# Performance work log

Hardware: AMD Instinct MI355X
Metric: run time of the kernel (lower is better)

Reference implementation:

```python
import jax, jax.numpy as jnp
import numpy as np

N = 50000
E = 800000
DIN = 128
DOUT = 128
T = 4  # number of edge types: onset, consecutive, during, rest


def setup_inputs() -> dict:
    key = jax.random.key(0)
    ks = jax.random.split(key, 12)
    s = 1.0 / np.sqrt(DIN)
    inp = {
        "x": jax.random.normal(ks[0], (N, DIN), dtype=jnp.float32),
        "edge_index": jax.random.randint(ks[1], (2, E), 0, N, dtype=jnp.int32),
        "edge_type": jax.random.randint(ks[2], (E,), 0, T, dtype=jnp.int32),
        # stacked per-etype parameters of ResGatedGraphConv
        "Wk": jax.random.uniform(ks[3], (T, DIN, DOUT), jnp.float32, -s, s),
        "bk": jax.random.uniform(ks[4], (T, DOUT), jnp.float32, -s, s),
        "Wq": jax.random.uniform(ks[5], (T, DIN, DOUT), jnp.float32, -s, s),
        "bq": jax.random.uniform(ks[6], (T, DOUT), jnp.float32, -s, s),
        "Wv": jax.random.uniform(ks[7], (T, DIN, DOUT), jnp.float32, -s, s),
        "bv": jax.random.uniform(ks[8], (T, DOUT), jnp.float32, -s, s),
        "Ws": jax.random.uniform(ks[9], (T, DIN, DOUT), jnp.float32, -s, s),
        "b": jax.random.uniform(ks[10], (T, DOUT), jnp.float32, -s, s),
    }
    return inp


def reference(x, edge_index, edge_type, Wk, bk, Wq, bq, Wv, bv, Ws, b):
    # PyG ResGatedGraphConv per edge type t, with edges masked to that type:
    #   out_i = sum_{j->i, type==t} sigmoid(k_i + q_j) * v_j + Ws_t x_i + b_t
    # followed by mean over edge types ('mean' reduction).
    src = edge_index[0]  # j (message source)
    dst = edge_index[1]  # i (message target)
    n = x.shape[0]
    outs = []
    for t in range(T):
        k = x @ Wk[t] + bk[t]  # [N, DOUT]
        q = x @ Wq[t] + bq[t]
        v = x @ Wv[t] + bv[t]
        eta = jax.nn.sigmoid(k[dst] + q[src])        # [E, DOUT]
        msg = eta * v[src]                            # [E, DOUT]
        msg = jnp.where((edge_type == t)[:, None], msg, 0.0)
        agg = jax.ops.segment_sum(msg, dst, num_segments=n)
        outs.append(agg + x @ Ws[t] + b[t])
    return jnp.mean(jnp.stack(outs, axis=0), axis=0)  # [N, DOUT]
```

## Files before the change

### kernel.cpp

```cpp
#include <hip/hip_runtime.h>

typedef unsigned short u16;
typedef unsigned int u32;
typedef __attribute__((ext_vector_type(8))) short bf16x8;
typedef __attribute__((ext_vector_type(4))) float f32x4;
typedef __attribute__((ext_vector_type(2))) float f32x2;
typedef __attribute__((ext_vector_type(4))) u16 u16x4;
typedef __attribute__((ext_vector_type(2))) u32 u32x2;
typedef __attribute__((ext_vector_type(4), aligned(4))) u32 u32x4a;
typedef __attribute__((ext_vector_type(2), aligned(4))) u32 u32x2a;

#define DIM 128
#define ROWB 2304
#define QV_SPAN 384
#define K_OFF 1536
#define S_OFF 2048
#define AS1C(p) ((const __attribute__((address_space(1))) void*)(p))
#define AS3P(p) ((__attribute__((address_space(3))) void*)(p))

#define QKSCALE -1.44269504088896341f

#if defined(__has_builtin)
#if __has_builtin(__builtin_amdgcn_exp2f)
#define EXP2(x) __builtin_amdgcn_exp2f(x)
#endif
#endif
#ifndef EXP2
extern "C" __device__ float __ocml_exp2_f32(float);
#define EXP2(x) __ocml_exp2_f32(x)
#endif

__device__ __forceinline__ u32 f2bf(float f){
  u32 x = __float_as_uint(f);
  return (x + 0x7fffu + ((x >> 16) & 1u)) >> 16;
}
__device__ __forceinline__ float bf2f(u16 u){
  return __uint_as_float(((u32)u) << 16);
}

__global__ __launch_bounds__(256) void prep_kernel(
    const float* __restrict__ x, u16* __restrict__ xb,
    const int* __restrict__ dst, int* __restrict__ cnt, int* __restrict__ rank,
    const float* __restrict__ Wk, const float* __restrict__ bk,
    const float* __restrict__ Wq, const float* __restrict__ bq,
    const float* __restrict__ Wv, const float* __restrict__ bv,
    const float* __restrict__ Ws, const float* __restrict__ bb,
    u16* __restrict__ WcatT, float* __restrict__ biascat,
    int T, int N, int E, int rows){
  int id = blockIdx.x * 256 + threadIdx.x;
  if (id < E){
    rank[id] = atomicAdd(&cnt[dst[id]], 1);
    return;
  }
  id -= E;
  int total_w = (3 * T + 1) * DIM * DIM;
  if (id < total_w){
    int kk = id & (DIM - 1);
    int c  = id >> 7;
    int nt = c >> 7;
    int j  = c & (DIM - 1);
    float wv, bvv;
    if (nt < T)        { wv = Wq[(nt*DIM + kk)*DIM + j] * QKSCALE;       bvv = bq[nt*DIM + j] * QKSCALE; }
    else if (nt < 2*T) { wv = Wv[((nt-T)*DIM + kk)*DIM + j];             bvv = bv[(nt-T)*DIM + j]; }
    else if (nt < 3*T) { wv = Wk[((nt-2*T)*DIM + kk)*DIM + j] * QKSCALE; bvv = bk[(nt-2*T)*DIM + j] * QKSCALE; }
    else {
      float s = 0.f, sb = 0.f;
      for (int t = 0; t < T; ++t){ s += Ws[(t*DIM + kk)*DIM + j]; sb += bb[t*DIM + j]; }
      wv = s / (float)T; bvv = sb / (float)T;
    }
    WcatT[(size_t)c * DIM + kk] = (u16)f2bf(wv);
    if (kk == 0) biascat[c] = bvv;
    return;
  }
  id -= total_w;
  int total_cast = rows * (DIM / 4);
  if (id < total_cast){
    int el = id * 4;
    int node = el >> 7;
    u32x2 pk;
    if (node < N){
      f32x4 v = *(const f32x4*)(x + el);
      pk.x = f2bf(v.x) | (f2bf(v.y) << 16);
      pk.y = f2bf(v.z) | (f2bf(v.w) << 16);
    } else { pk.x = 0u; pk.y = 0u; }
    *(u32x2*)(xb + el) = pk;
  }
}

__global__ __launch_bounds__(256) void scan1_kernel(const int* __restrict__ cnt,
                                                    int* __restrict__ offs,
                                                    int* __restrict__ bsum, int n){
  __shared__ int wsum[4];
  const int tid = threadIdx.x;
  const int lane = tid & 63, wave = tid >> 6;
  const int base = blockIdx.x * 2048 + tid * 8;
  int v[8]; int tot = 0;
#pragma unroll
  for (int j = 0; j < 8; ++j){
    int idx = base + j;
    int val = (idx < n) ? cnt[idx] : 0;
    v[j] = val; tot += val;
  }
  int incl = tot;
#pragma unroll
  for (int d = 1; d < 64; d <<= 1){
    int u = __shfl_up(incl, d, 64);
    if (lane >= d) incl += u;
  }
  if (lane == 63) wsum[wave] = incl;
  __syncthreads();
  int wbase = 0;
#pragma unroll
  for (int w = 0; w < 4; ++w) if (w < wave) wbase += wsum[w];
  int excl = wbase + incl - tot;
  if (tid == 255) bsum[blockIdx.x] = wbase + incl;
#pragma unroll
  for (int j = 0; j < 8; ++j){
    int idx = base + j;
    if (idx < n) offs[idx] = excl;
    excl += v[j];
  }
}

__global__ __launch_bounds__(64) void scan2_kernel(const int* __restrict__ bsum,
                                                   int* __restrict__ boffs, int nb,
                                                   int* __restrict__ packed, int E){
  int lane = threadIdx.x;
  int v = (lane < nb) ? bsum[lane] : 0;
  int incl = v;
#pragma unroll
  for (int d = 1; d < 64; d <<= 1){
    int u = __shfl_up(incl, d, 64);
    if (lane >= d) incl += u;
  }
  if (lane < nb) boffs[lane] = incl - v;
  if (lane < 8) packed[E + lane] = 0;
}

__global__ __launch_bounds__(256, 4) void gemm_scatter_kernel(
    const u16* __restrict__ xb, const u16* __restrict__ WcatT,
    const float* __restrict__ biascat, char* __restrict__ Y,
    const int* __restrict__ src, const int* __restrict__ dst,
    const int* __restrict__ et, const int* __restrict__ offs,
    const int* __restrict__ boffs, const int* __restrict__ rank,
    int* __restrict__ packed,
    int N, int E, int T, int NB, int mtiles, int nsc){
  __shared__ u16 wt[DIM * DIM];
  int bid = blockIdx.x;
  if (bid < nsc){
    int e = bid * 256 + threadIdx.x;
    if (e < E){
      int d = dst[e];
      int pos = offs[d] + boffs[d >> 11] + rank[e];
      int t = et[e] & 3;
      packed[pos] = src[e] * ROWB + t * QV_SPAN + (t << 28);
    }
    return;
  }
  bid -= nsc;
  int body = NB * (mtiles & ~7);
  int mt, nt;
  if (bid < body){
    int g = bid >> 3, r = bid & 7;
    int a = g / NB;
    mt = a * 8 + r;
    nt = g - a * NB;
  } else {
    int z = bid - body;
    mt = (mtiles & ~7) + z / NB;
    nt = z % NB;
  }
  const int m0 = mt * 128;
  const int n0 = nt * 128;
  const int tid  = threadIdx.x;
  const int wave = tid >> 6;
  const int lane = tid & 63;
  const int l15  = lane & 15;
  const int quad = lane >> 4;
  const int wrow = wave * 32;

  const u16* xrow0 = xb + (size_t)(m0 + wrow + l15) * DIM + quad * 8;
  const u16* xrow1 = xrow0 + 16 * DIM;

  bf16x8 bfr[2][4];
#pragma unroll
  for (int ks = 0; ks < 4; ++ks){
    bfr[0][ks] = *(const bf16x8*)(xrow0 + ks * 32);
    bfr[1][ks] = *(const bf16x8*)(xrow1 + ks * 32);
  }

#pragma unroll
  for (int it = 0; it < 8; ++it){
    int s  = it * 256 + tid;
    int r  = s >> 4;
    int p  = s & 15;
    int lb = p ^ (r & 7);
    int lbase = (it * 256 + wave * 64) * 8;
    __builtin_amdgcn_global_load_lds(AS1C(WcatT + (size_t)(n0 + r) * DIM + lb * 8),
                                     AS3P(wt + lbase), 16, 0, 0);
  }
  __syncthreads();

  f32x4 acc[2][8];
#pragma unroll
  for (int m = 0; m < 2; ++m)
#pragma unroll
    for (int f = 0; f < 8; ++f)
      acc[m][f] = (f32x4){0.f, 0.f, 0.f, 0.f};

#pragma unroll
  for (int ks = 0; ks < 4; ++ks){
    const int pb8 = (((ks * 4 + quad) ^ (l15 & 7)) * 8);
#pragma unroll
    for (int f = 0; f < 8; ++f){
      bf16x8 afr = *(const bf16x8*)&wt[(f * 16 + l15) * DIM + pb8];
      acc[0][f] = __builtin_amdgcn_mfma_f32_16x16x32_bf16(afr, bfr[0][ks], acc[0][f], 0, 0, 0);
      acc[1][f] = __builtin_amdgcn_mfma_f32_16x16x32_bf16(afr, bfr[1][ks], acc[1][f], 0, 0, 0);
    }
  }

  __syncthreads();
  char* lds = (char*)wt;
  const bool is_q = (nt < T);
  const bool is_k = (nt >= 2*T) && (nt < 3*T);
  if (is_q || is_k){
    const int boffb = is_q ? (nt * QV_SPAN) : (K_OFF + (nt - 2*T) * 128);
#pragma unroll
    for (int m = 0; m < 2; ++m){
      const int nl = wrow + m * 16 + l15;
#pragma unroll
      for (int f = 0; f < 8; ++f){
        const int feat = f * 16 + quad * 4;
        f32x4 b4 = *(const f32x4*)&biascat[n0 + feat];
        f32x4 v  = acc[m][f];
        u32 w = __builtin_amdgcn_cvt_pk_fp8_f32(v.x + b4.x, v.y + b4.y, 0, false);
        w = __builtin_amdgcn_cvt_pk_fp8_f32(v.z + b4.z, v.w + b4.w, w, true);
        *(u32*)(lds + nl * 128 + (feat ^ ((nl & 7) << 4))) = w;
      }
    }
    __syncthreads();
    const int seg = tid & 7;
    const int nr0 = tid >> 3;
#pragma unroll
    for (int pass = 0; pass < 4; ++pass){
      const int nl = pass * 32 + nr0;
      f32x4 d = *(const f32x4*)(lds + nl * 128 + ((seg ^ (nl & 7)) << 4));
      *(f32x4*)(Y + (size_t)(m0 + nl) * ROWB + boffb + seg * 16) = d;
    }
  } else {
    const int boffb = (nt < 2*T) ? ((nt - T) * QV_SPAN + 128) : S_OFF;
#pragma unroll
    for (int m = 0; m < 2; ++m){
      const int nl = wrow + m * 16 + l15;
#pragma unroll
      for (int f = 0; f < 8; ++f){
        const int feat = f * 16 + quad * 4;
        f32x4 b4 = *(const f32x4*)&biascat[n0 + feat];
        f32x4 v  = acc[m][f];
        u32 lo = f2bf(v.x + b4.x) | (f2bf(v.y + b4.y) << 16);
        u32 hi = f2bf(v.z + b4.z) | (f2bf(v.w + b4.w) << 16);
        u32x2 pk = {lo, hi};
        *(u32x2*)(lds + nl * 256 + ((feat * 2) ^ ((nl & 7) << 4))) = pk;
      }
    }
    __syncthreads();
    const int seg = tid & 15;
    const int nr0 = tid >> 4;
#pragma unroll
    for (int pass = 0; pass < 8; ++pass){
      const int nl = pass * 16 + nr0;
      f32x4 d = *(const f32x4*)(lds + nl * 256 + ((seg ^ (nl & 7)) << 4));
      *(f32x4*)(Y + (size_t)(m0 + nl) * ROWB + boffb + seg * 16) = d;
    }
  }
}

__global__ __launch_bounds__(256) void agg_kernel(const char* __restrict__ Y,
                                                  const int* __restrict__ offs,
                                                  const int* __restrict__ boffs,
                                                  const int* __restrict__ packed,
                                                  float* __restrict__ out,
                                                  int N, int E, float invT){
  __shared__ float klds[4 * 4 * 128];
  const int wave = threadIdx.x >> 6;
  const int lane = threadIdx.x & 63;
  const int node = blockIdx.x * 4 + wave;
  const bool valid = node < N;
  const int nc = valid ? node : N - 1;

  const char* yr = Y + (size_t)nc * ROWB;

  float* kwp = klds + wave * 512 + lane * 2;
#pragma unroll
  for (int t = 0; t < 4; ++t){
    u32 kw = *(const u16*)(yr + K_OFF + t * 128 + lane * 2);
    f32x2 kt2 = (f32x2){ __builtin_amdgcn_cvt_f32_fp8(kw, 0),
                         __builtin_amdgcn_cvt_f32_fp8(kw, 1) };
    *(f32x2*)(kwp + t * 128) = kt2;
  }
  u32 sw = *(const u32*)(yr + S_OFF + lane * 4);

  int e0 = 0, e1 = 0;
  if (valid){
    e0 = offs[nc] + boffs[nc >> 11];
    e1 = (nc == N - 1) ? E : (offs[nc + 1] + boffs[(nc + 1) >> 11]);
  }
  const u32 ql = (u32)(lane << 1);
  const u32 vl = (u32)(128 + (lane << 2));
  const char* kbase = (const char*)klds + wave * 2048 + (lane << 3);

  f32x2 acc2 = {0.f, 0.f};
  const int d = e1 - e0;
  if (d > 0){
    const int nb = (d + 5) / 6;
    u32 pA[6], vA[6], pB[6], vB[6];
    u32 qA[6], qB[6];

#define LOADI(P, Q, V, BI) do {                                        \
      const int* pp = packed + e0 + (BI) * 6;                          \
      u32x4a p4 = *(const u32x4a*)pp;                                  \
      u32x2a p2 = *(const u32x2a*)(pp + 4);                            \
      P[0] = p4.x; P[1] = p4.y; P[2] = p4.z; P[3] = p4.w;              \
      P[4] = p2.x; P[5] = p2.y;                                        \
      _Pragma("unroll")                                                \
      for (int j = 0; j < 6; ++j){                                     \
        u32 b = P[j] & 0x07FFFFFFu;                                    \
        Q[j] = (u32)(*(const u16*)(Y + b + ql));                       \
        V[j] = *(const u32*)(Y + b + vl);                              \
      }                                                                \
    } while(0)

#define COMP(P, Q, V, BI) do {                                         \
      int _eb = e0 + (BI) * 6;                                         \
      _Pragma("unroll")                                                \
      for (int j = 0; j < 6; ++j){                                     \
        f32x2 kt = *(const f32x2*)(kbase + ((P[j] >> 19) & 0x600u));   \
        u32 vv = (_eb + j < e1) ? V[j] : 0u;                           \
        f32x2 qf = __builtin_amdgcn_cvt_pk_f32_fp8(Q[j], false);       \
        f32x2 xx = kt + qf;                                            \
        f32x2 den = (f32x2){ 1.f + EXP2(xx.x), 1.f + EXP2(xx.y) };     \
        f32x2 g = (f32x2){ __builtin_amdgcn_rcpf(den.x),               \
                           __builtin_amdgcn_rcpf(den.y) };             \
        f32x2 vf = (f32x2){ __uint_as_float(vv << 16),                 \
                            __uint_as_float(vv & 0xffff0000u) };       \
        acc2 += g * vf;                                                \
      }                                                                \
    } while(0)

    LOADI(pA, qA, vA, 0);
    if (nb > 1) LOADI(pB, qB, vB, 1);
    int bi = 0;
    while (true){
      COMP(pA, qA, vA, bi);
      if (bi + 2 < nb) LOADI(pA, qA, vA, bi + 2);
      if (bi + 1 >= nb) break;
      COMP(pB, qB, vB, bi + 1);
      if (bi + 3 < nb) LOADI(pB, qB, vB, bi + 3);
      bi += 2;
      if (bi >= nb) break;
    }
#undef LOADI
#undef COMP
  }
  if (valid){
    f32x2 o = { invT * acc2.x + bf2f((u16)(sw & 0xffffu)),
                invT * acc2.y + bf2f((u16)(sw >> 16)) };
    *(f32x2*)&out[(size_t)node * DIM + lane * 2] = o;
  }
}

extern "C" void kernel_launch(void* const* d_in, const int* in_sizes, int n_in,
                              void* d_out, int out_size, void* d_ws, size_t ws_size,
                              hipStream_t stream){
  const float* x  = (const float*)d_in[0];
  const int*   ei = (const int*)d_in[1];
  const int*   et = (const int*)d_in[2];
  const float* Wk = (const float*)d_in[3];
  const float* bk = (const float*)d_in[4];
  const float* Wq = (const float*)d_in[5];
  const float* bq = (const float*)d_in[6];
  const float* Wv = (const float*)d_in[7];
  const float* bv = (const float*)d_in[8];
  const float* Ws = (const float*)d_in[9];
  const float* bb = (const float*)d_in[10];
  float* out = (float*)d_out;

  const int N = in_sizes[0] / DIM;
  const int E = in_sizes[2];
  const int T = in_sizes[3] / (DIM * DIM);
  const int NB = 3 * T + 1;
  const int ncol = NB * DIM;
  const int mtiles = (N + 127) / 128;
  const int rows = mtiles * 128;
  const int nscan = (N + 2047) / 2048;
  const int nsc = (E + 255) / 256;

  char* ws = (char*)d_ws;
  size_t off = 0;
  auto alloc = [&](size_t bytes) -> char* {
    char* p = ws + off;
    off = (off + bytes + 255) & ~(size_t)255;
    return p;
  };
  u16*   xb      = (u16*)alloc((size_t)rows * DIM * 2);
  u16*   WcatT   = (u16*)alloc((size_t)ncol * DIM * 2);
  float* biascat = (float*)alloc((size_t)ncol * 4);
  char*  Y       = (char*)alloc((size_t)rows * ROWB);
  int*   cnt     = (int*)alloc((size_t)N * 4);
  int*   offs    = (int*)alloc((size_t)N * 4);
  int*   rank    = (int*)alloc((size_t)E * 4);
  int*   packed  = (int*)alloc((size_t)(E + 8) * 4);
  int*   bsum    = (int*)alloc((size_t)nscan * 4);
  int*   boffs   = (int*)alloc((size_t)nscan * 4);
  (void)ws_size; (void)n_in; (void)out_size;

  const int* srcp = ei;
  const int* dstp = ei + E;

  hipMemsetAsync(cnt, 0, (size_t)N * 4, stream);
  int prep_total = E + NB * DIM * DIM + rows * (DIM / 4);
  prep_kernel<<<(prep_total + 255) / 256, 256, 0, stream>>>(
      x, xb, dstp, cnt, rank, Wk, bk, Wq, bq, Wv, bv, Ws, bb,
      WcatT, biascat, T, N, E, rows);
  scan1_kernel<<<nscan, 256, 0, stream>>>(cnt, offs, bsum, N);
  scan2_kernel<<<1, 64, 0, stream>>>(bsum, boffs, nscan, packed, E);
  gemm_scatter_kernel<<<nsc + NB * mtiles, 256, 0, stream>>>(
      xb, WcatT, biascat, Y, srcp, dstp, et, offs, boffs, rank, packed,
      N, E, T, NB, mtiles, nsc);
  agg_kernel<<<(N + 3) / 4, 256, 0, stream>>>(Y, offs, boffs, packed, out, N, E, 1.0f / (float)T);
}
```

Before: 250.2 us.

## Fuse all pipeline stages into one persistent cooperative kernel with grid syncs

Replaces the memset plus five separate launches (prep, two scans, gemm/scatter, aggregation) with a single cooperative persistent kernel. The stages are separated by grid.sync, and each stage walks its work with a grid-stride loop. The second-level scan is recomputed per block into LDS. The goal is to remove launch gaps and inter-kernel drain/fill overhead. In exchange, the grid is limited to the number of co-resident blocks (launch_bounds 256,4), grid barriers add cost, and there is less parallel slack in the heavy gemm and aggregation phases. If the cooperative launch fails, it falls back to the old multi-kernel path.

```diff
diff --git a/kernel.cpp b/kernel.cpp
--- a/kernel.cpp
+++ b/kernel.cpp
@@ -1,4 +1,7 @@
 #include <hip/hip_runtime.h>
+#include <hip/hip_cooperative_groups.h>
+
+namespace cg = cooperative_groups;
 
 typedef unsigned short u16;
 typedef unsigned int u32;
@@ -36,6 +39,348 @@
 }
 __device__ __forceinline__ float bf2f(u16 u){
   return __uint_as_float(((u32)u) << 16);
+}
+
+__global__ __launch_bounds__(256, 4) void fused_kernel(
+    const float* __restrict__ x, const int* __restrict__ srcp,
+    const int* __restrict__ dstp, const int* __restrict__ et,
+    const float* __restrict__ Wk, const float* __restrict__ bk,
+    const float* __restrict__ Wq, const float* __restrict__ bq,
+    const float* __restrict__ Wv, const float* __restrict__ bv,
+    const float* __restrict__ Ws, const float* __restrict__ bb,
+    u16* __restrict__ xb, u16* __restrict__ WcatT,
+    float* __restrict__ biascat, char* __restrict__ Y,
+    int* __restrict__ cnt, int* __restrict__ offs, int* __restrict__ rank,
+    int* __restrict__ packed, int* __restrict__ bsum,
+    float* __restrict__ out,
+    int N, int E, int T, int NB, int mtiles, int nsc,
+    int nscan, int rows, float invT){
+  __shared__ __align__(16) char smem[33024];
+  cg::grid_group grid = cg::this_grid();
+  const int tid = threadIdx.x;
+  const int G = gridDim.x;
+
+  for (int i = blockIdx.x * 256 + tid; i < N; i += G * 256) cnt[i] = 0;
+  grid.sync();
+
+  {
+    const int total_w = NB * DIM * DIM;
+    const int prep_total = E + total_w + rows * (DIM / 4);
+    for (int id0 = blockIdx.x * 256 + tid; id0 < prep_total; id0 += G * 256){
+      int id = id0;
+      if (id < E){
+        rank[id] = atomicAdd(&cnt[dstp[id]], 1);
+      } else {
+        id -= E;
+        if (id < total_w){
+          int kk = id & (DIM - 1);
+          int c  = id >> 7;
+          int nt = c >> 7;
+          int j  = c & (DIM - 1);
+          float wv, bvv;
+          if (nt < T)        { wv = Wq[(nt*DIM + kk)*DIM + j] * QKSCALE;       bvv = bq[nt*DIM + j] * QKSCALE; }
+          else if (nt < 2*T) { wv = Wv[((nt-T)*DIM + kk)*DIM + j];             bvv = bv[(nt-T)*DIM + j]; }
+          else if (nt < 3*T) { wv = Wk[((nt-2*T)*DIM + kk)*DIM + j] * QKSCALE; bvv = bk[(nt-2*T)*DIM + j] * QKSCALE; }
+          else {
+            float s = 0.f, sb = 0.f;
+            for (int t = 0; t < T; ++t){ s += Ws[(t*DIM + kk)*DIM + j]; sb += bb[t*DIM + j]; }
+            wv = s / (float)T; bvv = sb / (float)T;
+          }
+          WcatT[(size_t)c * DIM + kk] = (u16)f2bf(wv);
+          if (kk == 0) biascat[c] = bvv;
+        } else {
+          id -= total_w;
+          int el = id * 4;
+          int node = el >> 7;
+          u32x2 pk;
+          if (node < N){
+            f32x4 v = *(const f32x4*)(x + el);
+            pk.x = f2bf(v.x) | (f2bf(v.y) << 16);
+            pk.y = f2bf(v.z) | (f2bf(v.w) << 16);
+          } else { pk.x = 0u; pk.y = 0u; }
+          *(u32x2*)(xb + el) = pk;
+        }
+      }
+    }
+  }
+  grid.sync();
+
+  {
+    if (blockIdx.x == 0 && tid < 8) packed[E + tid] = 0;
+    int* wsum = (int*)(smem + 32768);
+    const int lane = tid & 63, wave = tid >> 6;
+    for (int cb = blockIdx.x; cb < nscan; cb += G){
+      const int base = cb * 2048 + tid * 8;
+      int v[8]; int tot = 0;
+#pragma unroll
+      for (int j = 0; j < 8; ++j){
+        int idx = base + j;
+        int val = (idx < N) ? cnt[idx] : 0;
+        v[j] = val; tot += val;
+      }
+      int incl = tot;
+#pragma unroll
+      for (int d = 1; d < 64; d <<= 1){
+        int u = __shfl_up(incl, d, 64);
+        if (lane >= d) incl += u;
+      }
+      if (lane == 63) wsum[wave] = incl;
+      __syncthreads();
+      int wbase = 0;
+#pragma unroll
+      for (int w = 0; w < 4; ++w) if (w < wave) wbase += wsum[w];
+      int excl = wbase + incl - tot;
+      if (tid == 255) bsum[cb] = wbase + incl;
+#pragma unroll
+      for (int j = 0; j < 8; ++j){
+        int idx = base + j;
+        if (idx < N) offs[idx] = excl;
+        excl += v[j];
+      }
+      __syncthreads();
+    }
+  }
+  grid.sync();
+
+  {
+    int* boffs_l = (int*)(smem + 32768);
+    if (tid < 64){
+      int v = (tid < nscan) ? bsum[tid] : 0;
+      int incl = v;
+#pragma unroll
+      for (int d = 1; d < 64; d <<= 1){
+        int u = __shfl_up(incl, d, 64);
+        if (tid >= d) incl += u;
+      }
+      if (tid < nscan) boffs_l[tid] = incl - v;
+    }
+    __syncthreads();
+
+    u16* wt = (u16*)smem;
+    const int tiles = NB * mtiles;
+    const int body = NB * (mtiles & ~7);
+    for (int vb = blockIdx.x; vb < nsc + tiles; vb += G){
+      if (vb < nsc){
+        int e = vb * 256 + tid;
+        if (e < E){
+          int d = dstp[e];
+          int pos = offs[d] + boffs_l[d >> 11] + rank[e];
+          int t = et[e] & 3;
+          packed[pos] = srcp[e] * ROWB + t * QV_SPAN + (t << 28);
+        }
+        continue;
+      }
+      int bid = vb - nsc;
+      int mt, nt;
+      if (bid < body){
+        int g = bid >> 3, r = bid & 7;
+        int a = g / NB;
+        mt = a * 8 + r;
+        nt = g - a * NB;
+      } else {
+        int z = bid - body;
+        mt = (mtiles & ~7) + z / NB;
+        nt = z % NB;
+      }
+      const int m0 = mt * 128;
+      const int n0 = nt * 128;
+      const int wave = tid >> 6;
+      const int lane = tid & 63;
+      const int l15  = lane & 15;
+      const int quad = lane >> 4;
+      const int wrow = wave * 32;
+
+      const u16* xrow0 = xb + (size_t)(m0 + wrow + l15) * DIM + quad * 8;
+      const u16* xrow1 = xrow0 + 16 * DIM;
+
+      bf16x8 bfr[2][4];
+#pragma unroll
+      for (int ks = 0; ks < 4; ++ks){
+        bfr[0][ks] = *(const bf16x8*)(xrow0 + ks * 32);
+        bfr[1][ks] = *(const bf16x8*)(xrow1 + ks * 32);
+      }
+
+      __syncthreads();
+#pragma unroll
+      for (int it = 0; it < 8; ++it){
+        int s  = it * 256 + tid;
+        int r  = s >> 4;
+        int p  = s & 15;
+        int lb = p ^ (r & 7);
+        int lbase = (it * 256 + wave * 64) * 8;
+        __builtin_amdgcn_global_load_lds(AS1C(WcatT + (size_t)(n0 + r) * DIM + lb * 8),
+                                         AS3P(wt + lbase), 16, 0, 0);
+      }
+      __syncthreads();
+
+      f32x4 acc[2][8];
+#pragma unroll
+      for (int m = 0; m < 2; ++m)
+#pragma unroll
+        for (int f = 0; f < 8; ++f)
+          acc[m][f] = (f32x4){0.f, 0.f, 0.f, 0.f};
+
+#pragma unroll
+      for (int ks = 0; ks < 4; ++ks){
+        const int pb8 = (((ks * 4 + quad) ^ (l15 & 7)) * 8);
+#pragma unroll
+        for (int f = 0; f < 8; ++f){
+          bf16x8 afr = *(const bf16x8*)&wt[(f * 16 + l15) * DIM + pb8];
+          acc[0][f] = __builtin_amdgcn_mfma_f32_16x16x32_bf16(afr, bfr[0][ks], acc[0][f], 0, 0, 0);
+          acc[1][f] = __builtin_amdgcn_mfma_f32_16x16x32_bf16(afr, bfr[1][ks], acc[1][f], 0, 0, 0);
+        }
+      }
+
+      __syncthreads();
+      char* lds = (char*)wt;
+      const bool is_q = (nt < T);
+      const bool is_k = (nt >= 2*T) && (nt < 3*T);
+      if (is_q || is_k){
+        const int boffb = is_q ? (nt * QV_SPAN) : (K_OFF + (nt - 2*T) * 128);
+#pragma unroll
+        for (int m = 0; m < 2; ++m){
+          const int nl = wrow + m * 16 + l15;
+#pragma unroll
+          for (int f = 0; f < 8; ++f){
+            const int feat = f * 16 + quad * 4;
+            f32x4 b4 = *(const f32x4*)&biascat[n0 + feat];
+            f32x4 v  = acc[m][f];
+            u32 w = __builtin_amdgcn_cvt_pk_fp8_f32(v.x + b4.x, v.y + b4.y, 0, false);
+            w = __builtin_amdgcn_cvt_pk_fp8_f32(v.z + b4.z, v.w + b4.w, w, true);
+            *(u32*)(lds + nl * 128 + (feat ^ ((nl & 7) << 4))) = w;
+          }
+        }
+        __syncthreads();
+        const int seg = tid & 7;
+        const int nr0 = tid >> 3;
+#pragma unroll
+        for (int pass = 0; pass < 4; ++pass){
+          const int nl = pass * 32 + nr0;
+          f32x4 d = *(const f32x4*)(lds + nl * 128 + ((seg ^ (nl & 7)) << 4));
+          *(f32x4*)(Y + (size_t)(m0 + nl) * ROWB + boffb + seg * 16) = d;
+        }
+      } else {
+        const int boffb = (nt < 2*T) ? ((nt - T) * QV_SPAN + 128) : S_OFF;
+#pragma unroll
+        for (int m = 0; m < 2; ++m){
+          const int nl = wrow + m * 16 + l15;
+#pragma unroll
+          for (int f = 0; f < 8; ++f){
+            const int feat = f * 16 + quad * 4;
+            f32x4 b4 = *(const f32x4*)&biascat[n0 + feat];
+            f32x4 v  = acc[m][f];
+            u32 lo = f2bf(v.x + b4.x) | (f2bf(v.y + b4.y) << 16);
+            u32 hi = f2bf(v.z + b4.z) | (f2bf(v.w + b4.w) << 16);
+            u32x2 pk = {lo, hi};
+            *(u32x2*)(lds + nl * 256 + ((feat * 2) ^ ((nl & 7) << 4))) = pk;
+          }
+        }
+        __syncthreads();
+        const int seg = tid & 15;
+        const int nr0 = tid >> 4;
+#pragma unroll
+        for (int pass = 0; pass < 8; ++pass){
+          const int nl = pass * 16 + nr0;
+          f32x4 d = *(const f32x4*)(lds + nl * 256 + ((seg ^ (nl & 7)) << 4));
+          *(f32x4*)(Y + (size_t)(m0 + nl) * ROWB + boffb + seg * 16) = d;
+        }
+      }
+    }
+  }
+  grid.sync();
+
+  {
+    float* klds = (float*)smem;
+    int* boffs_l = (int*)(smem + 32768);
+    const int wave = tid >> 6;
+    const int lane = tid & 63;
+    const int aggv = (N + 3) / 4;
+    const u32 ql = (u32)(lane << 1);
+    const u32 vl = (u32)(128 + (lane << 2));
+    const char* kbase = (const char*)klds + wave * 2048 + (lane << 3);
+    float* kwp = klds + wave * 512 + lane * 2;
+
+    for (int vb = blockIdx.x; vb < aggv; vb += G){
+      const int node = vb * 4 + wave;
+      const bool valid = node < N;
+      const int nc = valid ? node : N - 1;
+      const char* yr = Y + (size_t)nc * ROWB;
+
+#pragma unroll
+      for (int t = 0; t < 4; ++t){
+        u32 kw = *(const u16*)(yr + K_OFF + t * 128 + lane * 2);
+        f32x2 kt2 = (f32x2){ __builtin_amdgcn_cvt_f32_fp8(kw, 0),
+                             __builtin_amdgcn_cvt_f32_fp8(kw, 1) };
+        *(f32x2*)(kwp + t * 128) = kt2;
+      }
+      u32 sw = *(const u32*)(yr + S_OFF + lane * 4);
+
+      int e0 = 0, e1 = 0;
+      if (valid){
+        e0 = offs[nc] + boffs_l[nc >> 11];
+        e1 = (nc == N - 1) ? E : (offs[nc + 1] + boffs_l[(nc + 1) >> 11]);
+      }
+
+      f32x2 acc2 = {0.f, 0.f};
+      const int deg = e1 - e0;
+      if (deg > 0){
+        const int nb = (deg + 5) / 6;
+        u32 pA[6], vA[6], pB[6], vB[6];
+        u32 qA[6], qB[6];
+
+#define LOADI(P, Q, V, BI) do {                                        \
+        const int* pp = packed + e0 + (BI) * 6;                        \
+        u32x4a p4 = *(const u32x4a*)pp;                                \
+        u32x2a p2 = *(const u32x2a*)(pp + 4);                          \
+        P[0] = p4.x; P[1] = p4.y; P[2] = p4.z; P[3] = p4.w;            \
+        P[4] = p2.x; P[5] = p2.y;                                      \
+        _Pragma("unroll")                                              \
+        for (int j = 0; j < 6; ++j){                                   \
+          u32 b = P[j] & 0x07FFFFFFu;                                  \
+          Q[j] = (u32)(*(const u16*)(Y + b + ql));                     \
+          V[j] = *(const u32*)(Y + b + vl);                            \
+        }                                                              \
+      } while(0)
+
+#define COMP(P, Q, V, BI) do {                                         \
+        int _eb = e0 + (BI) * 6;                                       \
+        _Pragma("unroll")                                              \
+        for (int j = 0; j < 6; ++j){                                   \
+          f32x2 kt = *(const f32x2*)(kbase + ((P[j] >> 19) & 0x600u)); \
+          u32 vv = (_eb + j < e1) ? V[j] : 0u;                         \
+          f32x2 qf = __builtin_amdgcn_cvt_pk_f32_fp8(Q[j], false);     \
+          f32x2 xx = kt + qf;                                          \
+          f32x2 den = (f32x2){ 1.f + EXP2(xx.x), 1.f + EXP2(xx.y) };   \
+          f32x2 g = (f32x2){ __builtin_amdgcn_rcpf(den.x),             \
+                             __builtin_amdgcn_rcpf(den.y) };           \
+          f32x2 vf = (f32x2){ __uint_as_float(vv << 16),               \
+                              __uint_as_float(vv & 0xffff0000u) };     \
+          acc2 += g * vf;                                              \
+        }                                                              \
+      } while(0)
+
+        LOADI(pA, qA, vA, 0);
+        if (nb > 1) LOADI(pB, qB, vB, 1);
+        int bi = 0;
+        while (true){
+          COMP(pA, qA, vA, bi);
+          if (bi + 2 < nb) LOADI(pA, qA, vA, bi + 2);
+          if (bi + 1 >= nb) break;
+          COMP(pB, qB, vB, bi + 1);
+          if (bi + 3 < nb) LOADI(pB, qB, vB, bi + 3);
+          bi += 2;
+          if (bi >= nb) break;
+        }
+#undef LOADI
+#undef COMP
+      }
+      if (valid){
+        f32x2 o = { invT * acc2.x + bf2f((u16)(sw & 0xffffu)),
+                    invT * acc2.y + bf2f((u16)(sw >> 16)) };
+        *(f32x2*)&out[(size_t)node * DIM + lane * 2] = o;
+      }
+    }
+  }
 }
 
 __global__ __launch_bounds__(256) void prep_kernel(
@@ -289,7 +634,6 @@
   const int nc = valid ? node : N - 1;
 
   const char* yr = Y + (size_t)nc * ROWB;
-
   float* kwp = klds + wave * 512 + lane * 2;
 #pragma unroll
   for (int t = 0; t < 4; ++t){
@@ -385,15 +729,16 @@
   const float* bb = (const float*)d_in[10];
   float* out = (float*)d_out;
 
-  const int N = in_sizes[0] / DIM;
-  const int E = in_sizes[2];
-  const int T = in_sizes[3] / (DIM * DIM);
-  const int NB = 3 * T + 1;
+  int N = in_sizes[0] / DIM;
+  int E = in_sizes[2];
+  int T = in_sizes[3] / (DIM * DIM);
+  int NB = 3 * T + 1;
   const int ncol = NB * DIM;
-  const int mtiles = (N + 127) / 128;
-  const int rows = mtiles * 128;
-  const int nscan = (N + 2047) / 2048;
-  const int nsc = (E + 255) / 256;
+  int mtiles = (N + 127) / 128;
+  int rows = mtiles * 128;
+  int nscan = (N + 2047) / 2048;
+  int nsc = (E + 255) / 256;
+  float invT = 1.0f / (float)T;
 
   char* ws = (char*)d_ws;
   size_t off = 0;
@@ -417,15 +762,47 @@
   const int* srcp = ei;
   const int* dstp = ei + E;
 
-  hipMemsetAsync(cnt, 0, (size_t)N * 4, stream);
-  int prep_total = E + NB * DIM * DIM + rows * (DIM / 4);
-  prep_kernel<<<(prep_total + 255) / 256, 256, 0, stream>>>(
-      x, xb, dstp, cnt, rank, Wk, bk, Wq, bq, Wv, bv, Ws, bb,
-      WcatT, biascat, T, N, E, rows);
-  scan1_kernel<<<nscan, 256, 0, stream>>>(cnt, offs, bsum, N);
-  scan2_kernel<<<1, 64, 0, stream>>>(bsum, boffs, nscan, packed, E);
-  gemm_scatter_kernel<<<nsc + NB * mtiles, 256, 0, stream>>>(
-      xb, WcatT, biascat, Y, srcp, dstp, et, offs, boffs, rank, packed,
-      N, E, T, NB, mtiles, nsc);
-  agg_kernel<<<(N + 3) / 4, 256, 0, stream>>>(Y, offs, boffs, packed, out, N, E, 1.0f / (float)T);
+  static int G = 0;
+  if (G == 0){
+    int dev = 0;
+    (void)hipGetDevice(&dev);
+    int mp = 0;
+    (void)hipDeviceGetAttribute(&mp, hipDeviceAttributeMultiprocessorCount, dev);
+    int nb = 0;
+    (void)hipOccupancyMaxActiveBlocksPerMultiprocessor(&nb, fused_kernel, 256, 0);
+    if (mp <= 0) mp = 256;
+    if (nb <= 0) nb = 1;
+    G = mp * nb;
+    if (G > 8192) G = 8192;
+    G &= ~7;
+    if (G < 8) G = 8;
+  }
+
+  void* args[] = {
+    (void*)&x, (void*)&srcp, (void*)&dstp, (void*)&et,
+    (void*)&Wk, (void*)&bk, (void*)&Wq, (void*)&bq,
+    (void*)&Wv, (void*)&bv, (void*)&Ws, (void*)&bb,
+    (void*)&xb, (void*)&WcatT, (void*)&biascat, (void*)&Y,
+    (void*)&cnt, (void*)&offs, (void*)&rank, (void*)&packed, (void*)&bsum,
+    (void*)&out,
+    (void*)&N, (void*)&E, (void*)&T, (void*)&NB, (void*)&mtiles, (void*)&nsc,
+    (void*)&nscan, (void*)&rows, (void*)&invT
+  };
+
+  hipError_t err = hipLaunchCooperativeKernel(fused_kernel, dim3(G), dim3(256),
+                                              args, 0, stream);
+  if (err != hipSuccess){
+    (void)hipGetLastError();
+    hipMemsetAsync(cnt, 0, (size_t)N * 4, stream);
+    int prep_total = E + NB * DIM * DIM + rows * (DIM / 4);
+    prep_kernel<<<(prep_total + 255) / 256, 256, 0, stream>>>(
+        x, xb, dstp, cnt, rank, Wk, bk, Wq, bq, Wv, bv, Ws, bb,
+        WcatT, biascat, T, N, E, rows);
+    scan1_kernel<<<nscan, 256, 0, stream>>>(cnt, offs, bsum, N);
+    scan2_kernel<<<1, 64, 0, stream>>>(bsum, boffs, nscan, packed, E);
+    gemm_scatter_kernel<<<nsc + NB * mtiles, 256, 0, stream>>>(
+        xb, WcatT, biascat, Y, srcp, dstp, et, offs, boffs, rank, packed,
+        N, E, T, NB, mtiles, nsc);
+    agg_kernel<<<(N + 3) / 4, 256, 0, stream>>>(Y, offs, boffs, packed, out, N, E, invT);
+  }
 }
```

Result: slower. 577.2 us (+130.7%).
